# Kernel optimization log

Hardware: AMD Instinct MI355X
Metric: run time of the kernel (lower is better)

## Reference

```python
import jax, jax.numpy as jnp
import numpy as np
from jax import lax

D_MODEL = 768
D_STATE = 16
D_CONV = 4
EXPAND = 2
D_INNER = EXPAND * D_MODEL  # 1536
DT_RANK = (D_MODEL + 15) // 16  # 48
BATCH = 4
SEQ_LEN = 2048


def setup_inputs() -> dict:
    key = jax.random.key(0)
    ks = jax.random.split(key, 8)
    x = jax.random.normal(ks[0], (BATCH, SEQ_LEN, D_MODEL), dtype=jnp.float32)
    W_in = jax.random.normal(ks[1], (D_INNER * 2, D_MODEL), dtype=jnp.float32) * 0.02
    conv_w = jax.random.normal(ks[2], (D_INNER, 1, D_CONV), dtype=jnp.float32) * 0.1
    conv_b = jnp.zeros((D_INNER,), dtype=jnp.float32)
    W_x = jax.random.normal(ks[3], (DT_RANK + 2 * D_STATE, D_INNER), dtype=jnp.float32) * 0.02
    dt_std = DT_RANK ** -0.5
    W_dt = jax.random.uniform(ks[4], (D_INNER, DT_RANK), minval=-dt_std, maxval=dt_std, dtype=jnp.float32)
    b_dt = jnp.zeros((D_INNER,), dtype=jnp.float32)
    A_log = jnp.log(jnp.tile(jnp.arange(1, D_STATE + 1, dtype=jnp.float32), (D_INNER, 1)))
    D_param = jnp.ones((D_INNER,), dtype=jnp.float32)
    W_out = jax.random.normal(ks[5], (D_MODEL, D_INNER), dtype=jnp.float32) * 0.02
    return {"x": x, "W_in": W_in, "conv_w": conv_w, "conv_b": conv_b,
            "W_x": W_x, "W_dt": W_dt, "b_dt": b_dt, "A_log": A_log,
            "D_param": D_param, "W_out": W_out}


def _silu(v):
    return v * jax.nn.sigmoid(v)


def reference(x, W_in, conv_w, conv_b, W_x, W_dt, b_dt, A_log, D_param, W_out):
    B, L, _ = x.shape
    # in_proj and split into x-branch / gate z
    xz = jnp.einsum('bld,ed->ble', x, W_in)            # (B, L, 2*d_inner)
    xb, z = jnp.split(xz, 2, axis=-1)
    # depthwise causal conv1d (torch pads both sides then truncates to L)
    xc = jnp.transpose(xb, (0, 2, 1))                   # (B, d_inner, L)
    xc = lax.conv_general_dilated(xc, conv_w, window_strides=(1,),
                                  padding=[(D_CONV - 1, 0)],
                                  feature_group_count=D_INNER,
                                  dimension_numbers=('NCH', 'OIH', 'NCH'))
    xc = xc + conv_b[None, :, None]
    xc = jnp.transpose(xc, (0, 2, 1))                   # (B, L, d_inner)
    xc = _silu(xc)
    # ssm input-dependent params
    x_dbl = jnp.einsum('bld,ed->ble', xc, W_x)          # (B, L, dt_rank+2*d_state)
    dt_r = x_dbl[..., :DT_RANK]
    Bm = x_dbl[..., DT_RANK:DT_RANK + D_STATE]          # (B, L, d_state)
    Cm = x_dbl[..., DT_RANK + D_STATE:]
    dt = jax.nn.softplus(jnp.einsum('blr,dr->bld', dt_r, W_dt) + b_dt)
    A = -jnp.exp(A_log)                                 # (d_inner, d_state)
    # selective scan over time
    def step(h, inp):
        x_t, dt_t, B_t, C_t = inp                       # (B,d_inner),(B,d_inner),(B,d_state),(B,d_state)
        dA = jnp.exp(dt_t[..., None] * A)               # (B, d_inner, d_state)
        h = dA * h + (dt_t * x_t)[..., None] * B_t[:, None, :]
        y_t = jnp.einsum('bdn,bn->bd', h, C_t) + D_param * x_t
        return h, y_t
    h0 = jnp.zeros((B, D_INNER, D_STATE), dtype=x.dtype)
    xs = (jnp.transpose(xc, (1, 0, 2)), jnp.transpose(dt, (1, 0, 2)),
          jnp.transpose(Bm, (1, 0, 2)), jnp.transpose(Cm, (1, 0, 2)))
    _, ys = lax.scan(step, h0, xs)                      # (L, B, d_inner)
    y = jnp.transpose(ys, (1, 0, 2))
    y = y * _silu(z)
    return jnp.einsum('bld,od->blo', y, W_out)
```

## Files before the change

kernel.cpp:

```cpp
#include <hip/hip_runtime.h>
#include <hip/hip_bf16.h>
#include <math.h>

#define D_MODEL   768
#define D_STATE   16
#define D_CONV    4
#define D_INNER   1536
#define DT_RANK   48
#define BATCH     4
#define SEQ_LEN   2048
#define BL        (BATCH * SEQ_LEN)
#define NCHUNK    32
#define CHUNK     (SEQ_LEN / NCHUNK)

typedef __bf16 bf16x8 __attribute__((ext_vector_type(8)));
typedef float  f32x4  __attribute__((ext_vector_type(4)));

__device__ __forceinline__ void async_copy16(const void* g, void* l) {
    __builtin_amdgcn_global_load_lds(
        (const __attribute__((address_space(1))) void*)g,
        (__attribute__((address_space(3))) void*)l,
        16, 0, 0);
}

template <int EPI>
__global__ __launch_bounds__(256)
void gemm_f(const __bf16* __restrict__ A, const __bf16* __restrict__ B,
            float* __restrict__ C, const float* __restrict__ bias,
            int M, int N, int K, int ldc)
{
    __shared__ __bf16 Asl[128 * 64];
    __shared__ __bf16 Bsl[128 * 64];

    const int tid  = threadIdx.x;
    const int lane = tid & 63;
    const int w    = tid >> 6;
    const int wm   = (w >> 1) * 64;
    const int wn   = (w & 1) * 64;

    const int bm = blockIdx.y * 128;
    const int bn = blockIdx.x * 128;

    const long lda = 2L * K;
    const long ldb = 2L * K;

    f32x4 acc[4][4];
    #pragma unroll
    for (int i = 0; i < 4; ++i)
        #pragma unroll
        for (int j = 0; j < 4; ++j)
            acc[i][j] = (f32x4){0.f, 0.f, 0.f, 0.f};

    const int srow = w * 32 + (lane >> 3);
    const int q    = (lane & 7) ^ ((lane >> 3) & 7);
    const int qoff = (q < 4) ? q * 8 : K + (q - 4) * 8;
    const __bf16* Abase = A + (long)(bm + srow) * lda + qoff;
    const __bf16* Bbase = B + (long)(bn + srow) * ldb + qoff;
    char* AslW = (char*)Asl + (w * 32) * 128;
    char* BslW = (char*)Bsl + (w * 32) * 128;

    const int fr = lane & 15;
    const int g4 = lane >> 4;
    const long lda8 = 8 * lda, ldb8 = 8 * ldb;

    for (int kk = 0; kk < K; kk += 32) {
        __syncthreads();
        #pragma unroll
        for (int j = 0; j < 4; ++j) {
            async_copy16(Abase + j * lda8 + kk, AslW + j * 1024);
            async_copy16(Bbase + j * ldb8 + kk, BslW + j * 1024);
        }
        __syncthreads();

        bf16x8 ah[4], al[4], bh[4], bl[4];
        #pragma unroll
        for (int t = 0; t < 4; ++t) {
            const int ra = wm + t * 16 + fr;
            const int rb = wn + t * 16 + fr;
            ah[t] = *(const bf16x8*)&Asl[ra * 64 + ((g4       ^ (ra & 7)) * 8)];
            al[t] = *(const bf16x8*)&Asl[ra * 64 + (((4 + g4) ^ (ra & 7)) * 8)];
            bh[t] = *(const bf16x8*)&Bsl[rb * 64 + ((g4       ^ (rb & 7)) * 8)];
            bl[t] = *(const bf16x8*)&Bsl[rb * 64 + (((4 + g4) ^ (rb & 7)) * 8)];
        }
        #pragma unroll
        for (int i = 0; i < 4; ++i)
            #pragma unroll
            for (int j = 0; j < 4; ++j) {
                acc[i][j] = __builtin_amdgcn_mfma_f32_16x16x32_bf16(ah[i], bh[j], acc[i][j], 0, 0, 0);
                acc[i][j] = __builtin_amdgcn_mfma_f32_16x16x32_bf16(ah[i], bl[j], acc[i][j], 0, 0, 0);
                acc[i][j] = __builtin_amdgcn_mfma_f32_16x16x32_bf16(al[i], bh[j], acc[i][j], 0, 0, 0);
            }
    }

    const int cn  = lane & 15;
    const int cr4 = (lane >> 4) * 4;
    #pragma unroll
    for (int i = 0; i < 4; ++i)
        #pragma unroll
        for (int j = 0; j < 4; ++j)
            #pragma unroll
            for (int r = 0; r < 4; ++r) {
                const int row = bm + wm + i * 16 + cr4 + r;
                const int col = bn + wn + j * 16 + cn;
                float v = acc[i][j][r];
                if (EPI == 1) {
                    v += bias[col];
                    v = fmaxf(v, 0.f) + log1pf(__expf(-fabsf(v)));
                }
                C[(long)row * ldc + col] = v;
            }
}

__global__ __launch_bounds__(256)
void gemm_xdbl(const __bf16* __restrict__ A, const __bf16* __restrict__ B,
               float* __restrict__ Pout)
{
    __shared__ __bf16 Asl[128 * 64];
    __shared__ __bf16 Bsl[128 * 64];

    const int tid  = threadIdx.x;
    const int lane = tid & 63;
    const int w    = tid >> 6;
    const int wm   = (w >> 1) * 64;
    const int wn   = (w & 1) * 64;

    const int s  = blockIdx.x;
    const int bm = blockIdx.y * 128;
    const int K  = 1536;
    const long lda = 3072, ldb = 3072;

    f32x4 acc[4][4];
    #pragma unroll
    for (int i = 0; i < 4; ++i)
        #pragma unroll
        for (int j = 0; j < 4; ++j)
            acc[i][j] = (f32x4){0.f, 0.f, 0.f, 0.f};

    const int srow = w * 32 + (lane >> 3);
    const int q    = (lane & 7) ^ ((lane >> 3) & 7);
    const int qoff = (q < 4) ? q * 8 : K + (q - 4) * 8;
    const __bf16* Abase = A + (long)(bm + srow) * lda + qoff;
    const __bf16* Bbase = B + (long)srow * ldb + qoff;
    char* AslW = (char*)Asl + (w * 32) * 128;
    char* BslW = (char*)Bsl + (w * 32) * 128;

    const int fr = lane & 15;
    const int g4 = lane >> 4;
    const long lda8 = 8 * lda, ldb8 = 8 * ldb;

    for (int kt = s * 12; kt < (s + 1) * 12; ++kt) {
        const int kk = kt * 32;
        __syncthreads();
        #pragma unroll
        for (int j = 0; j < 4; ++j) {
            async_copy16(Abase + j * lda8 + kk, AslW + j * 1024);
            async_copy16(Bbase + j * ldb8 + kk, BslW + j * 1024);
        }
        __syncthreads();

        bf16x8 ah[4], al[4], bh[4], bl[4];
        #pragma unroll
        for (int t = 0; t < 4; ++t) {
            const int ra = wm + t * 16 + fr;
            const int rb = wn + t * 16 + fr;
            ah[t] = *(const bf16x8*)&Asl[ra * 64 + ((g4       ^ (ra & 7)) * 8)];
            al[t] = *(const bf16x8*)&Asl[ra * 64 + (((4 + g4) ^ (ra & 7)) * 8)];
            bh[t] = *(const bf16x8*)&Bsl[rb * 64 + ((g4       ^ (rb & 7)) * 8)];
            bl[t] = *(const bf16x8*)&Bsl[rb * 64 + (((4 + g4) ^ (rb & 7)) * 8)];
        }
        #pragma unroll
        for (int i = 0; i < 4; ++i)
            #pragma unroll
            for (int j = 0; j < 4; ++j) {
                acc[i][j] = __builtin_amdgcn_mfma_f32_16x16x32_bf16(ah[i], bh[j], acc[i][j], 0, 0, 0);
                acc[i][j] = __builtin_amdgcn_mfma_f32_16x16x32_bf16(ah[i], bl[j], acc[i][j], 0, 0, 0);
                acc[i][j] = __builtin_amdgcn_mfma_f32_16x16x32_bf16(al[i], bh[j], acc[i][j], 0, 0, 0);
            }
    }

    float* Cp = Pout + (long)s * (8192L * 128);
    const int cn  = lane & 15;
    const int cr4 = (lane >> 4) * 4;
    #pragma unroll
    for (int i = 0; i < 4; ++i)
        #pragma unroll
        for (int j = 0; j < 4; ++j)
            #pragma unroll
            for (int r = 0; r < 4; ++r) {
                const int row = bm + wm + i * 16 + cr4 + r;
                const int col = wn + j * 16 + cn;
                Cp[(long)row * 128 + col] = acc[i][j][r];
            }
}

__global__ __launch_bounds__(256)
void xdbl_reduce3(const float* __restrict__ Pout, float* __restrict__ xbc,
                  __bf16* __restrict__ xdtS)
{
    const long i = (long)blockIdx.x * 256 + threadIdx.x;
    if (i >= 8192L * 128) return;
    const long r  = i >> 7;
    const int  c  = (int)(i & 127);
    const long st = 8192L * 128;
    const long rb = r * 128;

    const int k = c & 63;
    float u = 0.f;
    if (k < 48) {
        const long o = rb + k;
        u = (Pout[o] + Pout[o + st]) + (Pout[o + 2 * st] + Pout[o + 3 * st]);
    }
    const __bf16 hi = (__bf16)u;
    xdtS[rb + c] = (c < 64) ? hi : (__bf16)(u - (float)hi);

    if (c >= 96) {
        const int j = c - 96;
        const long o = rb + 48 + j;
        xbc[r * 32 + j] =
            (Pout[o] + Pout[o + st]) + (Pout[o + 2 * st] + Pout[o + 3 * st]);
    }
}

#define NW0 ((long)BL * 768)
#define NW1 (3072L * 768)
#define NW2 (768L * 1536)
#define NW3 (80L * 1536)
#define NW4 (1536L * 128)
__global__ __launch_bounds__(256)
void split_all(const float* __restrict__ x,
               const float* __restrict__ W_in, const float* __restrict__ W_out,
               const float* __restrict__ W_x, const float* __restrict__ W_dt,
               __bf16* __restrict__ xS,
               __bf16* __restrict__ wInS, __bf16* __restrict__ wOutS,
               __bf16* __restrict__ wXS, __bf16* __restrict__ wDtS)
{
    long i = (long)blockIdx.x * 256 + threadIdx.x;
    if (i < NW0) {
        const long row = i / 768; const int col = (int)(i - row * 768);
        const float a = x[i];
        const __bf16 h = (__bf16)a;
        __bf16* d = xS + row * 1536 + col;
        d[0] = h; d[768] = (__bf16)(a - (float)h);
        return;
    }
    i -= NW0;
    if (i < NW1) {
        const long row = i / 768; const int col = (int)(i - row * 768);
        const float a = W_in[i];
        const __bf16 h = (__bf16)a;
        __bf16* d = wInS + row * 1536 + col;
        d[0] = h; d[768] = (__bf16)(a - (float)h);
        return;
    }
    i -= NW1;
    if (i < NW2) {
        const long row = i / 1536; const int col = (int)(i - row * 1536);
        const float a = W_out[i];
        const __bf16 h = (__bf16)a;
        __bf16* d = wOutS + row * 3072 + col;
        d[0] = h; d[1536] = (__bf16)(a - (float)h);
        return;
    }
    i -= NW2;
    if (i < NW3) {
        const long row = i / 1536; const int col = (int)(i - row * 1536);
        const float a = W_x[i];
        const __bf16 h = (__bf16)a;
        __bf16* d = wXS + row * 3072 + col;
        d[0] = h; d[1536] = (__bf16)(a - (float)h);
        return;
    }
    i -= NW3;
    if (i < NW4) {
        const long row = i >> 7; const int c = (int)(i & 127);
        const int k = c & 63;
        const float a = (k < 48) ? W_dt[row * 48 + k] : 0.f;
        const __bf16 h = (__bf16)a;
        wDtS[row * 128 + c] = (c < 64) ? h : (__bf16)(a - (float)h);
    }
}

__global__ __launch_bounds__(256)
void conv_silu_kernel(const float* __restrict__ xz,
                      const float* __restrict__ conv_w,
                      const float* __restrict__ conv_b,
                      __bf16* __restrict__ xcS)
{
    const long idx = (long)blockIdx.x * 256 + threadIdx.x;
    const int d  = (int)(idx % D_INNER);
    const long bl = idx / D_INNER;
    const int l  = (int)(bl % SEQ_LEN);

    const float w0 = conv_w[d * 4 + 0];
    const float w1 = conv_w[d * 4 + 1];
    const float w2 = conv_w[d * 4 + 2];
    const float w3 = conv_w[d * 4 + 3];

    const float* base = xz + bl * 3072 + d;
    float s = conv_b[d];
    if (l >= 3) s = fmaf(base[-3 * 3072], w0, s);
    if (l >= 2) s = fmaf(base[-2 * 3072], w1, s);
    if (l >= 1) s = fmaf(base[-1 * 3072], w2, s);
    s = fmaf(base[0], w3, s);
    const float sig = 1.f / (1.f + __expf(-s));
    const float v = s * sig;
    const __bf16 hi = (__bf16)v;
    const __bf16 lo = (__bf16)(v - (float)hi);
    xcS[bl * 3072 + d]        = hi;
    xcS[bl * 3072 + 1536 + d] = lo;
}

__global__ __launch_bounds__(256)
void scan_phaseA(const __bf16* __restrict__ xcS, const float* __restrict__ xz,
                 const float* __restrict__ xbc, const float* __restrict__ A_log,
                 float* __restrict__ P, float* __restrict__ S)
{
    const int d = blockIdx.x * 256 + threadIdx.x;
    const int c = blockIdx.y;
    const int b = blockIdx.z;

    float An[16], Pr[16], Sr[16];
    #pragma unroll
    for (int n = 0; n < 16; ++n) {
        An[n] = -__expf(A_log[d * 16 + n]);
        Pr[n] = 1.f;
        Sr[n] = 0.f;
    }

    const long bl0 = (long)b * SEQ_LEN + (long)c * CHUNK;
    for (int l = 0; l < CHUNK; ++l) {
        const long bl = bl0 + l;
        const float dt  = xz[bl * 3072 + d];
        const float x   = (float)xcS[bl * 3072 + d] + (float)xcS[bl * 3072 + 1536 + d];
        const float dtx = dt * x;
        const float* bc = xbc + bl * 32;
        #pragma unroll
        for (int n = 0; n < 16; ++n) {
            const float a = __expf(dt * An[n]);
            Pr[n] *= a;
            Sr[n] = fmaf(a, Sr[n], dtx * bc[n]);
        }
    }

    const long base = ((long)(b * NCHUNK + c) * 16) * D_INNER + d;
    #pragma unroll
    for (int n = 0; n < 16; ++n) {
        P[base + (long)n * D_INNER] = Pr[n];
        S[base + (long)n * D_INNER] = Sr[n];
    }
}

__global__ __launch_bounds__(256)
void scan_phaseB(const float* __restrict__ P, const float* __restrict__ S,
                 float* __restrict__ H)
{
    const int t = blockIdx.x * 256 + threadIdx.x;
    const int d = t % D_INNER;
    const int r = t / D_INNER;
    const int n = r & 15;
    const int b = r >> 4;

    float h = 0.f;
    for (int c = 0; c < NCHUNK; ++c) {
        const long i = ((long)(b * NCHUNK + c) * 16 + n) * D_INNER + d;
        H[i] = h;
        h = fmaf(P[i], h, S[i]);
    }
}

__global__ __launch_bounds__(256)
void scan_phaseC(__bf16* xcS_yS, const float* __restrict__ xz,
                 const float* __restrict__ xbc, const float* __restrict__ A_log,
                 const float* __restrict__ Dp, const float* __restrict__ H)
{
    const int d = blockIdx.x * 256 + threadIdx.x;
    const int c = blockIdx.y;
    const int b = blockIdx.z;

    float An[16], h[16];
    const long hbase = ((long)(b * NCHUNK + c) * 16) * D_INNER + d;
    #pragma unroll
    for (int n = 0; n < 16; ++n) {
        An[n] = -__expf(A_log[d * 16 + n]);
        h[n]  = H[hbase + (long)n * D_INNER];
    }
    const float Dd = Dp[d];

    const long bl0 = (long)b * SEQ_LEN + (long)c * CHUNK;
    for (int l = 0; l < CHUNK; ++l) {
        const long bl = bl0 + l;
        const float dt  = xz[bl * 3072 + d];
        const float x   = (float)xcS_yS[bl * 3072 + d] + (float)xcS_yS[bl * 3072 + 1536 + d];
        const float dtx = dt * x;
        const float* bc = xbc + bl * 32;
        float y = Dd * x;
        #pragma unroll
        for (int n = 0; n < 16; ++n) {
            const float a = __expf(dt * An[n]);
            h[n] = fmaf(a, h[n], dtx * bc[n]);
            y = fmaf(h[n], bc[16 + n], y);
        }
        const float z  = xz[bl * 3072 + D_INNER + d];
        const float sz = z / (1.f + __expf(-z));
        const float v  = y * sz;
        const __bf16 hi = (__bf16)v;
        const __bf16 lo = (__bf16)(v - (float)hi);
        xcS_yS[bl * 3072 + d]        = hi;
        xcS_yS[bl * 3072 + 1536 + d] = lo;
    }
}

extern "C" void kernel_launch(void* const* d_in, const int* in_sizes, int n_in,
                              void* d_out, int out_size, void* d_ws, size_t ws_size,
                              hipStream_t stream)
{
    const float* x      = (const float*)d_in[0];
    const float* W_in   = (const float*)d_in[1];
    const float* conv_w = (const float*)d_in[2];
    const float* conv_b = (const float*)d_in[3];
    const float* W_x    = (const float*)d_in[4];
    const float* W_dt   = (const float*)d_in[5];
    const float* b_dt   = (const float*)d_in[6];
    const float* A_log  = (const float*)d_in[7];
    const float* D_p    = (const float*)d_in[8];
    const float* W_out  = (const float*)d_in[9];
    float* out = (float*)d_out;

    char* p = (char*)d_ws;
    auto take = [&](size_t bytes) { char* r = p; p += (bytes + 255) & ~(size_t)255; return r; };

    float*  xz    = (float*)take((size_t)BL * 3072 * 4);
    float*  H     = (float*)take((size_t)BATCH * NCHUNK * 16 * D_INNER * 4);
    __bf16* wOutS = (__bf16*)take(768L * 3072 * 2);
    __bf16* wXS   = (__bf16*)take(128L * 3072 * 2);
    __bf16* wDtS  = (__bf16*)take(1536L * 128 * 2);
    __bf16* xdtS  = (__bf16*)take(8192L * 128 * 2);
    float*  xbc   = (float*)take(8192L * 32 * 4);
    float*  Pout  = (float*)take(4L * 8192 * 128 * 4);
    float*  S     = (float*)take((size_t)BATCH * NCHUNK * 16 * D_INNER * 4);
    float*  P     = Pout;

    char* region = take(50331648);
    __bf16* xS   = (__bf16*)region;
    __bf16* wInS = (__bf16*)(region + 25165824);
    __bf16* xcS  = (__bf16*)region;
    __bf16* yS   = (__bf16*)region;

    {
        const long n = NW0 + NW1 + NW2 + NW3 + NW4;
        split_all<<<(int)((n + 255) / 256), 256, 0, stream>>>(
            x, W_in, W_out, W_x, W_dt, xS, wInS, wOutS, wXS, wDtS);
    }
    {
        dim3 grid(3072 / 128, BL / 128);
        gemm_f<0><<<grid, 256, 0, stream>>>(xS, wInS, xz, nullptr,
                                            BL, 3072, 768, 3072);
    }
    {
        const long total = (long)BL * D_INNER;
        conv_silu_kernel<<<(int)(total / 256), 256, 0, stream>>>(xz, conv_w, conv_b, xcS);
    }
    {
        dim3 grid(4, BL / 128);
        gemm_xdbl<<<grid, 256, 0, stream>>>(xcS, wXS, Pout);
    }
    {
        const long n = 8192L * 128;
        xdbl_reduce3<<<(int)((n + 255) / 256), 256, 0, stream>>>(Pout, xbc, xdtS);
    }
    {
        dim3 grid(1536 / 128, BL / 128);
        gemm_f<1><<<grid, 256, 0, stream>>>(xdtS, wDtS, xz, b_dt,
                                            BL, 1536, 64, 3072);
    }
    {
        dim3 grid(D_INNER / 256, NCHUNK, BATCH);
        scan_phaseA<<<grid, 256, 0, stream>>>(xcS, xz, xbc, A_log, P, S);
    }
    scan_phaseB<<<(BATCH * 16 * D_INNER) / 256, 256, 0, stream>>>(P, S, H);
    {
        dim3 grid(D_INNER / 256, NCHUNK, BATCH);
        scan_phaseC<<<grid, 256, 0, stream>>>(xcS, xz, xbc, A_log, D_p, H);
    }
    {
        dim3 grid(768 / 128, BL / 128);
        gemm_f<0><<<grid, 256, 0, stream>>>(yS, wOutS, out, nullptr,
                                            BL, 768, 1536, 768);
    }
}
```

Baseline: 530.8 us.

## Double-buffer LDS tiles in split-bf16 GEMMs to overlap loads with MFMA

Both the generic GEMM and the x_dbl GEMM now use two LDS buffers, issuing async global-to-LDS copies for the next K-tile before running the MFMAs on the current one. The old sync-load-sync-compute pattern is replaced by a vmcnt wait plus a barrier, and s_setprio is raised around the MFMA block. The intent is to hide global load latency behind compute, at the cost of doubling LDS use (64KB per block), which may reduce occupancy. The loop assumes an even tile count.

```diff
diff --git a/kernel.cpp b/kernel.cpp
--- a/kernel.cpp
+++ b/kernel.cpp
@@ -23,14 +23,60 @@
         16, 0, 0);
 }
 
+
+#define TILE_SYNC() do {                                    \
+    asm volatile("s_waitcnt vmcnt(0)" ::: "memory");        \
+    __builtin_amdgcn_s_barrier();                           \
+} while (0)
+
+__device__ __forceinline__ void tile_stage(const __bf16* Ab, const __bf16* Bb,
+                                           long lda8, long ldb8, int kk,
+                                           char* AslW, char* BslW)
+{
+    #pragma unroll
+    for (int j = 0; j < 4; ++j) {
+        async_copy16(Ab + j * lda8 + kk, AslW + j * 1024);
+        async_copy16(Bb + j * ldb8 + kk, BslW + j * 1024);
+    }
+    __builtin_amdgcn_sched_barrier(0);
+}
+
+__device__ __forceinline__ void tile_compute(const __bf16* Asl, const __bf16* Bsl,
+                                             int wm, int wn, int fr, int g4,
+                                             f32x4 (&acc)[4][4])
+{
+    bf16x8 ah[4], al[4], bh[4], bl[4];
+    #pragma unroll
+    for (int t = 0; t < 4; ++t) {
+        const int ra = wm + t * 16 + fr;
+        const int rb = wn + t * 16 + fr;
+        ah[t] = *(const bf16x8*)&Asl[ra * 64 + ((g4       ^ (ra & 7)) * 8)];
+        al[t] = *(const bf16x8*)&Asl[ra * 64 + (((4 + g4) ^ (ra & 7)) * 8)];
+        bh[t] = *(const bf16x8*)&Bsl[rb * 64 + ((g4       ^ (rb & 7)) * 8)];
+        bl[t] = *(const bf16x8*)&Bsl[rb * 64 + (((4 + g4) ^ (rb & 7)) * 8)];
+    }
+    __builtin_amdgcn_s_setprio(1);
+    #pragma unroll
+    for (int i = 0; i < 4; ++i)
+        #pragma unroll
+        for (int j = 0; j < 4; ++j) {
+            acc[i][j] = __builtin_amdgcn_mfma_f32_16x16x32_bf16(ah[i], bh[j], acc[i][j], 0, 0, 0);
+            acc[i][j] = __builtin_amdgcn_mfma_f32_16x16x32_bf16(ah[i], bl[j], acc[i][j], 0, 0, 0);
+            acc[i][j] = __builtin_amdgcn_mfma_f32_16x16x32_bf16(al[i], bh[j], acc[i][j], 0, 0, 0);
+        }
+    __builtin_amdgcn_s_setprio(0);
+}
+
 template <int EPI>
 __global__ __launch_bounds__(256)
 void gemm_f(const __bf16* __restrict__ A, const __bf16* __restrict__ B,
             float* __restrict__ C, const float* __restrict__ bias,
             int M, int N, int K, int ldc)
 {
-    __shared__ __bf16 Asl[128 * 64];
-    __shared__ __bf16 Bsl[128 * 64];
+    __shared__ __bf16 Asl0[128 * 64];
+    __shared__ __bf16 Bsl0[128 * 64];
+    __shared__ __bf16 Asl1[128 * 64];
+    __shared__ __bf16 Bsl1[128 * 64];
 
     const int tid  = threadIdx.x;
     const int lane = tid & 63;
@@ -56,40 +102,29 @@
     const int qoff = (q < 4) ? q * 8 : K + (q - 4) * 8;
     const __bf16* Abase = A + (long)(bm + srow) * lda + qoff;
     const __bf16* Bbase = B + (long)(bn + srow) * ldb + qoff;
-    char* AslW = (char*)Asl + (w * 32) * 128;
-    char* BslW = (char*)Bsl + (w * 32) * 128;
+    const int wb = (w * 32) * 128;
+    char* AslW0 = (char*)Asl0 + wb;
+    char* BslW0 = (char*)Bsl0 + wb;
+    char* AslW1 = (char*)Asl1 + wb;
+    char* BslW1 = (char*)Bsl1 + wb;
 
     const int fr = lane & 15;
     const int g4 = lane >> 4;
     const long lda8 = 8 * lda, ldb8 = 8 * ldb;
 
-    for (int kk = 0; kk < K; kk += 32) {
-        __syncthreads();
-        #pragma unroll
-        for (int j = 0; j < 4; ++j) {
-            async_copy16(Abase + j * lda8 + kk, AslW + j * 1024);
-            async_copy16(Bbase + j * ldb8 + kk, BslW + j * 1024);
-        }
-        __syncthreads();
-
-        bf16x8 ah[4], al[4], bh[4], bl[4];
-        #pragma unroll
-        for (int t = 0; t < 4; ++t) {
-            const int ra = wm + t * 16 + fr;
-            const int rb = wn + t * 16 + fr;
-            ah[t] = *(const bf16x8*)&Asl[ra * 64 + ((g4       ^ (ra & 7)) * 8)];
-            al[t] = *(const bf16x8*)&Asl[ra * 64 + (((4 + g4) ^ (ra & 7)) * 8)];
-            bh[t] = *(const bf16x8*)&Bsl[rb * 64 + ((g4       ^ (rb & 7)) * 8)];
-            bl[t] = *(const bf16x8*)&Bsl[rb * 64 + (((4 + g4) ^ (rb & 7)) * 8)];
-        }
-        #pragma unroll
-        for (int i = 0; i < 4; ++i)
-            #pragma unroll
-            for (int j = 0; j < 4; ++j) {
-                acc[i][j] = __builtin_amdgcn_mfma_f32_16x16x32_bf16(ah[i], bh[j], acc[i][j], 0, 0, 0);
-                acc[i][j] = __builtin_amdgcn_mfma_f32_16x16x32_bf16(ah[i], bl[j], acc[i][j], 0, 0, 0);
-                acc[i][j] = __builtin_amdgcn_mfma_f32_16x16x32_bf16(al[i], bh[j], acc[i][j], 0, 0, 0);
-            }
+    const int nt = K >> 5;
+
+    tile_stage(Abase, Bbase, lda8, ldb8, 0, AslW0, BslW0);
+    TILE_SYNC();
+
+    for (int tt = 0; tt < nt; tt += 2) {
+        tile_stage(Abase, Bbase, lda8, ldb8, (tt + 1) * 32, AslW1, BslW1);
+        tile_compute(Asl0, Bsl0, wm, wn, fr, g4, acc);
+        TILE_SYNC();
+        if (tt + 2 < nt)
+            tile_stage(Abase, Bbase, lda8, ldb8, (tt + 2) * 32, AslW0, BslW0);
+        tile_compute(Asl1, Bsl1, wm, wn, fr, g4, acc);
+        TILE_SYNC();
     }
 
     const int cn  = lane & 15;
@@ -115,8 +150,10 @@
 void gemm_xdbl(const __bf16* __restrict__ A, const __bf16* __restrict__ B,
                float* __restrict__ Pout)
 {
-    __shared__ __bf16 Asl[128 * 64];
-    __shared__ __bf16 Bsl[128 * 64];
+    __shared__ __bf16 Asl0[128 * 64];
+    __shared__ __bf16 Bsl0[128 * 64];
+    __shared__ __bf16 Asl1[128 * 64];
+    __shared__ __bf16 Bsl1[128 * 64];
 
     const int tid  = threadIdx.x;
     const int lane = tid & 63;
@@ -141,41 +178,29 @@
     const int qoff = (q < 4) ? q * 8 : K + (q - 4) * 8;
     const __bf16* Abase = A + (long)(bm + srow) * lda + qoff;
     const __bf16* Bbase = B + (long)srow * ldb + qoff;
-    char* AslW = (char*)Asl + (w * 32) * 128;
-    char* BslW = (char*)Bsl + (w * 32) * 128;
+    const int wb = (w * 32) * 128;
+    char* AslW0 = (char*)Asl0 + wb;
+    char* BslW0 = (char*)Bsl0 + wb;
+    char* AslW1 = (char*)Asl1 + wb;
+    char* BslW1 = (char*)Bsl1 + wb;
 
     const int fr = lane & 15;
     const int g4 = lane >> 4;
     const long lda8 = 8 * lda, ldb8 = 8 * ldb;
 
-    for (int kt = s * 12; kt < (s + 1) * 12; ++kt) {
-        const int kk = kt * 32;
-        __syncthreads();
-        #pragma unroll
-        for (int j = 0; j < 4; ++j) {
-            async_copy16(Abase + j * lda8 + kk, AslW + j * 1024);
-            async_copy16(Bbase + j * ldb8 + kk, BslW + j * 1024);
-        }
-        __syncthreads();
-
-        bf16x8 ah[4], al[4], bh[4], bl[4];
-        #pragma unroll
-        for (int t = 0; t < 4; ++t) {
-            const int ra = wm + t * 16 + fr;
-            const int rb = wn + t * 16 + fr;
-            ah[t] = *(const bf16x8*)&Asl[ra * 64 + ((g4       ^ (ra & 7)) * 8)];
-            al[t] = *(const bf16x8*)&Asl[ra * 64 + (((4 + g4) ^ (ra & 7)) * 8)];
-            bh[t] = *(const bf16x8*)&Bsl[rb * 64 + ((g4       ^ (rb & 7)) * 8)];
-            bl[t] = *(const bf16x8*)&Bsl[rb * 64 + (((4 + g4) ^ (rb & 7)) * 8)];
-        }
-        #pragma unroll
-        for (int i = 0; i < 4; ++i)
-            #pragma unroll
-            for (int j = 0; j < 4; ++j) {
-                acc[i][j] = __builtin_amdgcn_mfma_f32_16x16x32_bf16(ah[i], bh[j], acc[i][j], 0, 0, 0);
-                acc[i][j] = __builtin_amdgcn_mfma_f32_16x16x32_bf16(ah[i], bl[j], acc[i][j], 0, 0, 0);
-                acc[i][j] = __builtin_amdgcn_mfma_f32_16x16x32_bf16(al[i], bh[j], acc[i][j], 0, 0, 0);
-            }
+    const int k0 = s * 384;
+
+    tile_stage(Abase, Bbase, lda8, ldb8, k0, AslW0, BslW0);
+    TILE_SYNC();
+
+    for (int tt = 0; tt < 12; tt += 2) {
+        tile_stage(Abase, Bbase, lda8, ldb8, k0 + (tt + 1) * 32, AslW1, BslW1);
+        tile_compute(Asl0, Bsl0, wm, wn, fr, g4, acc);
+        TILE_SYNC();
+        if (tt + 2 < 12)
+            tile_stage(Abase, Bbase, lda8, ldb8, k0 + (tt + 2) * 32, AslW0, BslW0);
+        tile_compute(Asl1, Bsl1, wm, wn, fr, g4, acc);
+        TILE_SYNC();
     }
 
     float* Cp = Pout + (long)s * (8192L * 128);
```

After: 533.4 us. About the same (+0.5%).

## Triple-buffer GEMM loads with 128x192 tiles, 8 waves, and grid swizzle

Applied to the files above, without the earlier changes.

Rewrites the generic split-bf16 GEMM to use a three-stage LDS ring buffer. Async global-to-LDS copies for tile t+2 are issued while tile t is computed, replacing the two-barrier load-then-compute loop. The block grows to 512 threads with a 128x192 output tile, uses a workgroup index swizzle for L2 locality, and raises wave priority around the MFMA block. This aims to hide global load latency and reduce barrier stalls, at the cost of more LDS (about 120 KB) and tighter register and occupancy limits.

```diff
diff --git a/kernel.cpp b/kernel.cpp
--- a/kernel.cpp
+++ b/kernel.cpp
@@ -24,72 +24,108 @@
 }
 
 template <int EPI>
-__global__ __launch_bounds__(256)
+__global__ __launch_bounds__(512, 2)
 void gemm_f(const __bf16* __restrict__ A, const __bf16* __restrict__ B,
             float* __restrict__ C, const float* __restrict__ bias,
             int M, int N, int K, int ldc)
 {
-    __shared__ __bf16 Asl[128 * 64];
-    __shared__ __bf16 Bsl[128 * 64];
+    __shared__ __bf16 Asl[3][128 * 64];
+    __shared__ __bf16 Bsl[3][192 * 64];
 
     const int tid  = threadIdx.x;
     const int lane = tid & 63;
     const int w    = tid >> 6;
-    const int wm   = (w >> 1) * 64;
-    const int wn   = (w & 1) * 64;
-
-    const int bm = blockIdx.y * 128;
-    const int bn = blockIdx.x * 128;
+    const int wm   = (w >> 2) * 64;
+    const int wn   = (w & 3) * 48;
+
+    const int nwg  = gridDim.x * gridDim.y;
+    const int orig = blockIdx.x + gridDim.x * blockIdx.y;
+    const int swz  = (orig & 7) * (nwg >> 3) + (orig >> 3);
+    const int bn   = (swz % gridDim.x) * 192;
+    const int bm   = (swz / gridDim.x) * 128;
 
     const long lda = 2L * K;
     const long ldb = 2L * K;
 
-    f32x4 acc[4][4];
+    f32x4 acc[4][3];
     #pragma unroll
     for (int i = 0; i < 4; ++i)
         #pragma unroll
-        for (int j = 0; j < 4; ++j)
+        for (int j = 0; j < 3; ++j)
             acc[i][j] = (f32x4){0.f, 0.f, 0.f, 0.f};
 
-    const int srow = w * 32 + (lane >> 3);
-    const int q    = (lane & 7) ^ ((lane >> 3) & 7);
+    const int srow = w * 8 + (lane >> 3);
+    const int q    = (lane & 7) ^ (lane >> 3);
     const int qoff = (q < 4) ? q * 8 : K + (q - 4) * 8;
     const __bf16* Abase = A + (long)(bm + srow) * lda + qoff;
     const __bf16* Bbase = B + (long)(bn + srow) * ldb + qoff;
-    char* AslW = (char*)Asl + (w * 32) * 128;
-    char* BslW = (char*)Bsl + (w * 32) * 128;
+    const long lda64 = 64 * lda, ldb64 = 64 * ldb;
+    const int wboff = w * 1024;
 
     const int fr = lane & 15;
     const int g4 = lane >> 4;
-    const long lda8 = 8 * lda, ldb8 = 8 * ldb;
-
-    for (int kk = 0; kk < K; kk += 32) {
-        __syncthreads();
-        #pragma unroll
-        for (int j = 0; j < 4; ++j) {
-            async_copy16(Abase + j * lda8 + kk, AslW + j * 1024);
-            async_copy16(Bbase + j * ldb8 + kk, BslW + j * 1024);
-        }
-        __syncthreads();
-
-        bf16x8 ah[4], al[4], bh[4], bl[4];
+
+    const int nt = K >> 5;
+
+    auto STAGE = [&](int kk, int buf) {
+        char* Ad = (char*)Asl[buf] + wboff;
+        char* Bd = (char*)Bsl[buf] + wboff;
+        async_copy16(Abase + kk,             Ad);
+        async_copy16(Abase + kk + lda64,     Ad + 8192);
+        async_copy16(Bbase + kk,             Bd);
+        async_copy16(Bbase + kk + ldb64,     Bd + 8192);
+        async_copy16(Bbase + kk + 2 * ldb64, Bd + 16384);
+    };
+
+    auto COMPUTE = [&](int buf) {
+        const __bf16* As = Asl[buf];
+        const __bf16* Bs = Bsl[buf];
+        bf16x8 ah[4], al[4], bh[3], bl[3];
         #pragma unroll
         for (int t = 0; t < 4; ++t) {
             const int ra = wm + t * 16 + fr;
+            ah[t] = *(const bf16x8*)&As[ra * 64 + ((g4       ^ (ra & 7)) * 8)];
+            al[t] = *(const bf16x8*)&As[ra * 64 + (((4 + g4) ^ (ra & 7)) * 8)];
+        }
+        #pragma unroll
+        for (int t = 0; t < 3; ++t) {
             const int rb = wn + t * 16 + fr;
-            ah[t] = *(const bf16x8*)&Asl[ra * 64 + ((g4       ^ (ra & 7)) * 8)];
-            al[t] = *(const bf16x8*)&Asl[ra * 64 + (((4 + g4) ^ (ra & 7)) * 8)];
-            bh[t] = *(const bf16x8*)&Bsl[rb * 64 + ((g4       ^ (rb & 7)) * 8)];
-            bl[t] = *(const bf16x8*)&Bsl[rb * 64 + (((4 + g4) ^ (rb & 7)) * 8)];
+            bh[t] = *(const bf16x8*)&Bs[rb * 64 + ((g4       ^ (rb & 7)) * 8)];
+            bl[t] = *(const bf16x8*)&Bs[rb * 64 + (((4 + g4) ^ (rb & 7)) * 8)];
         }
+        __builtin_amdgcn_s_setprio(1);
         #pragma unroll
         for (int i = 0; i < 4; ++i)
             #pragma unroll
-            for (int j = 0; j < 4; ++j) {
+            for (int j = 0; j < 3; ++j) {
                 acc[i][j] = __builtin_amdgcn_mfma_f32_16x16x32_bf16(ah[i], bh[j], acc[i][j], 0, 0, 0);
                 acc[i][j] = __builtin_amdgcn_mfma_f32_16x16x32_bf16(ah[i], bl[j], acc[i][j], 0, 0, 0);
                 acc[i][j] = __builtin_amdgcn_mfma_f32_16x16x32_bf16(al[i], bh[j], acc[i][j], 0, 0, 0);
             }
+        __builtin_amdgcn_s_setprio(0);
+    };
+
+    auto ITER = [&](int t, int cb, int sb) {
+        if (t + 2 < nt) STAGE((t + 2) * 32, sb);
+        __builtin_amdgcn_sched_barrier(0);
+        COMPUTE(cb);
+        asm volatile("s_waitcnt lgkmcnt(0)" ::: "memory");
+        if (t + 2 < nt) asm volatile("s_waitcnt vmcnt(5)" ::: "memory");
+        else            asm volatile("s_waitcnt vmcnt(0)" ::: "memory");
+        __builtin_amdgcn_s_barrier();
+        __builtin_amdgcn_sched_barrier(0);
+    };
+
+    STAGE(0, 0);
+    STAGE(32, 1);
+    asm volatile("s_waitcnt vmcnt(5)" ::: "memory");
+    __builtin_amdgcn_s_barrier();
+    __builtin_amdgcn_sched_barrier(0);
+
+    for (int t = 0; t < nt; t += 3) {
+        ITER(t, 0, 2);
+        if (t + 1 < nt) ITER(t + 1, 1, 0);
+        if (t + 2 < nt) ITER(t + 2, 2, 1);
     }
 
     const int cn  = lane & 15;
@@ -97,7 +133,7 @@
     #pragma unroll
     for (int i = 0; i < 4; ++i)
         #pragma unroll
-        for (int j = 0; j < 4; ++j)
+        for (int j = 0; j < 3; ++j)
             #pragma unroll
             for (int r = 0; r < 4; ++r) {
                 const int row = bm + wm + i * 16 + cr4 + r;
@@ -452,8 +488,8 @@
             x, W_in, W_out, W_x, W_dt, xS, wInS, wOutS, wXS, wDtS);
     }
     {
-        dim3 grid(3072 / 128, BL / 128);
-        gemm_f<0><<<grid, 256, 0, stream>>>(xS, wInS, xz, nullptr,
+        dim3 grid(3072 / 192, BL / 128);
+        gemm_f<0><<<grid, 512, 0, stream>>>(xS, wInS, xz, nullptr,
                                             BL, 3072, 768, 3072);
     }
     {
@@ -469,8 +505,8 @@
         xdbl_reduce3<<<(int)((n + 255) / 256), 256, 0, stream>>>(Pout, xbc, xdtS);
     }
     {
-        dim3 grid(1536 / 128, BL / 128);
-        gemm_f<1><<<grid, 256, 0, stream>>>(xdtS, wDtS, xz, b_dt,
+        dim3 grid(1536 / 192, BL / 128);
+        gemm_f<1><<<grid, 512, 0, stream>>>(xdtS, wDtS, xz, b_dt,
                                             BL, 1536, 64, 3072);
     }
     {
@@ -483,8 +519,8 @@
         scan_phaseC<<<grid, 256, 0, stream>>>(xcS, xz, xbc, A_log, D_p, H);
     }
     {
-        dim3 grid(768 / 128, BL / 128);
-        gemm_f<0><<<grid, 256, 0, stream>>>(yS, wOutS, out, nullptr,
+        dim3 grid(768 / 192, BL / 128);
+        gemm_f<0><<<grid, 512, 0, stream>>>(yS, wOutS, out, nullptr,
                                             BL, 768, 1536, 768);
     }
 }
```

Result: slower. 548.6 us (+3.3%).

## Replace in_proj GEMM with 256x256-tile 8-wave double-buffered split-bf16 kernel

Applied to the files above, without the earlier changes.

Adds a new GEMM kernel for the in_proj matmul that uses 256x256 output tiles with 512 threads, double-buffered LDS filled by async global-to-LDS copies, and quarter-step interleaving of loads with MFMA work under fine-grained vmcnt waits and s_setprio. It keeps the three-product hi/lo bf16 split for near-fp32 accuracy. The larger tile is meant to raise arithmetic intensity and overlap memory with MFMA. In exchange it uses 128KB of LDS and many accumulator registers, which limits occupancy, and its epilogue does scalar stores.

```diff
diff --git a/kernel.cpp b/kernel.cpp
--- a/kernel.cpp
+++ b/kernel.cpp
@@ -21,6 +21,171 @@
         (const __attribute__((address_space(1))) void*)g,
         (__attribute__((address_space(3))) void*)l,
         16, 0, 0);
+}
+
+
+#define SYNC_V4 do { asm volatile("s_waitcnt vmcnt(4)" ::: "memory"); \
+    __builtin_amdgcn_s_barrier(); __builtin_amdgcn_sched_barrier(0); } while (0)
+#define SYNC_V2 do { asm volatile("s_waitcnt vmcnt(2)" ::: "memory"); \
+    __builtin_amdgcn_s_barrier(); __builtin_amdgcn_sched_barrier(0); } while (0)
+#define SYNC_V0 do { asm volatile("s_waitcnt vmcnt(0)" ::: "memory"); \
+    __builtin_amdgcn_s_barrier(); __builtin_amdgcn_sched_barrier(0); } while (0)
+
+template<int IH, int JH>
+__device__ __forceinline__ void quad24(f32x4 (&acc)[2][4][2][2],
+                                       const bf16x8 (&aH)[4], const bf16x8 (&aL)[4],
+                                       const bf16x8 (&bH)[2], const bf16x8 (&bL)[2])
+{
+    __builtin_amdgcn_s_setprio(1);
+    #pragma unroll
+    for (int i = 0; i < 4; ++i)
+        #pragma unroll
+        for (int j = 0; j < 2; ++j) {
+            acc[IH][i][JH][j] = __builtin_amdgcn_mfma_f32_16x16x32_bf16(aH[i], bH[j], acc[IH][i][JH][j], 0, 0, 0);
+            acc[IH][i][JH][j] = __builtin_amdgcn_mfma_f32_16x16x32_bf16(aH[i], bL[j], acc[IH][i][JH][j], 0, 0, 0);
+            acc[IH][i][JH][j] = __builtin_amdgcn_mfma_f32_16x16x32_bf16(aL[i], bH[j], acc[IH][i][JH][j], 0, 0, 0);
+        }
+    __builtin_amdgcn_s_setprio(0);
+}
+
+__global__ __launch_bounds__(512, 2)
+void gemm256(const __bf16* __restrict__ A, const __bf16* __restrict__ B,
+             float* __restrict__ C, int K, int ldc)
+{
+    __shared__ __bf16 Asl0[256 * 64];
+    __shared__ __bf16 Bsl0[256 * 64];
+    __shared__ __bf16 Asl1[256 * 64];
+    __shared__ __bf16 Bsl1[256 * 64];
+
+    const int tid  = threadIdx.x;
+    const int lane = tid & 63;
+    const int w    = tid >> 6;
+    const int aw   = (w >> 2) * 64;
+    const int bw   = (w & 3) * 32;
+
+    const int bm = blockIdx.y * 256;
+    const int bn = blockIdx.x * 256;
+
+    const long lda = 2L * K;
+    const long ldb = 2L * K;
+
+    f32x4 acc[2][4][2][2];
+    #pragma unroll
+    for (int a = 0; a < 2; ++a)
+        #pragma unroll
+        for (int i = 0; i < 4; ++i)
+            #pragma unroll
+            for (int b = 0; b < 2; ++b)
+                #pragma unroll
+                for (int j = 0; j < 2; ++j)
+                    acc[a][i][b][j] = (f32x4){0.f, 0.f, 0.f, 0.f};
+
+    const int srow = w * 8 + (lane >> 3);
+    const int q    = (lane & 7) ^ ((lane >> 3) & 7);
+    const int qoff = (q < 4) ? q * 8 : K + (q - 4) * 8;
+    const __bf16* Ab = A + (long)(bm + srow) * lda + qoff;
+    const __bf16* Bb = B + (long)(bn + srow) * ldb + qoff;
+    const long lda64 = 64 * lda, ldb64 = 64 * ldb;
+    const int wo = w * 1024;
+
+    const int fr = lane & 15;
+    const int g4 = lane >> 4;
+
+    const int nt = K >> 5;
+
+    __bf16 *Ac = Asl0, *Bc = Bsl0, *An = Asl1, *Bn = Bsl1;
+
+    auto stA = [&](int kk, __bf16* dst, int half) {
+        char* d = (char*)dst + half * 16384 + wo;
+        const __bf16* s = Ab + kk + (long)(2 * half) * lda64;
+        async_copy16(s, d);
+        async_copy16(s + lda64, d + 8192);
+    };
+    auto stB = [&](int kk, __bf16* dst, int half) {
+        char* d = (char*)dst + half * 16384 + wo;
+        const __bf16* s = Bb + kk + (long)(2 * half) * ldb64;
+        async_copy16(s, d);
+        async_copy16(s + ldb64, d + 8192);
+    };
+    auto rdA = [&](const __bf16* As, int ih, bf16x8 (&aH)[4], bf16x8 (&aL)[4]) {
+        #pragma unroll
+        for (int t = 0; t < 4; ++t) {
+            const int ra = aw + ih * 128 + t * 16 + fr;
+            aH[t] = *(const bf16x8*)&As[ra * 64 + ((g4       ^ (ra & 7)) * 8)];
+            aL[t] = *(const bf16x8*)&As[ra * 64 + (((4 + g4) ^ (ra & 7)) * 8)];
+        }
+    };
+    auto rdB = [&](const __bf16* Bs, int jh, bf16x8 (&bH)[2], bf16x8 (&bL)[2]) {
+        #pragma unroll
+        for (int t = 0; t < 2; ++t) {
+            const int rb = bw + jh * 128 + t * 16 + fr;
+            bH[t] = *(const bf16x8*)&Bs[rb * 64 + ((g4       ^ (rb & 7)) * 8)];
+            bL[t] = *(const bf16x8*)&Bs[rb * 64 + (((4 + g4) ^ (rb & 7)) * 8)];
+        }
+    };
+
+    stA(0, Ac, 0);
+    stB(0, Bc, 0);
+    stB(0, Bc, 1);
+    stA(0, Ac, 1);
+    SYNC_V4;
+
+    for (int t = 0; t < nt - 1; ++t) {
+        const int kk1 = (t + 1) * 32;
+        bf16x8 aH[4], aL[4], bH[2], bL[2];
+        rdA(Ac, 0, aH, aL);
+        rdB(Bc, 0, bH, bL);
+        stA(kk1, An, 0);
+        SYNC_V4;
+        quad24<0, 0>(acc, aH, aL, bH, bL);
+        rdB(Bc, 1, bH, bL);
+        stB(kk1, Bn, 0);
+        SYNC_V4;
+        quad24<0, 1>(acc, aH, aL, bH, bL);
+        rdA(Ac, 1, aH, aL);
+        stB(kk1, Bn, 1);
+        SYNC_V4;
+        quad24<1, 1>(acc, aH, aL, bH, bL);
+        rdB(Bc, 0, bH, bL);
+        stA(kk1, An, 1);
+        SYNC_V4;
+        quad24<1, 0>(acc, aH, aL, bH, bL);
+        __bf16* tp;
+        tp = Ac; Ac = An; An = tp;
+        tp = Bc; Bc = Bn; Bn = tp;
+    }
+
+    {
+        bf16x8 aH[4], aL[4], bH[2], bL[2];
+        rdA(Ac, 0, aH, aL);
+        rdB(Bc, 0, bH, bL);
+        SYNC_V2;
+        quad24<0, 0>(acc, aH, aL, bH, bL);
+        rdB(Bc, 1, bH, bL);
+        SYNC_V0;
+        quad24<0, 1>(acc, aH, aL, bH, bL);
+        rdA(Ac, 1, aH, aL);
+        quad24<1, 1>(acc, aH, aL, bH, bL);
+        rdB(Bc, 0, bH, bL);
+        quad24<1, 0>(acc, aH, aL, bH, bL);
+    }
+
+    const int cn  = lane & 15;
+    const int cr4 = (lane >> 4) * 4;
+    #pragma unroll
+    for (int ih = 0; ih < 2; ++ih)
+        #pragma unroll
+        for (int i = 0; i < 4; ++i)
+            #pragma unroll
+            for (int jh = 0; jh < 2; ++jh)
+                #pragma unroll
+                for (int j = 0; j < 2; ++j)
+                    #pragma unroll
+                    for (int r = 0; r < 4; ++r) {
+                        const int row = bm + aw + ih * 128 + i * 16 + cr4 + r;
+                        const int col = bn + bw + jh * 128 + j * 16 + cn;
+                        C[(long)row * ldc + col] = acc[ih][i][jh][j][r];
+                    }
 }
 
 template <int EPI>
@@ -452,9 +617,8 @@
             x, W_in, W_out, W_x, W_dt, xS, wInS, wOutS, wXS, wDtS);
     }
     {
-        dim3 grid(3072 / 128, BL / 128);
-        gemm_f<0><<<grid, 256, 0, stream>>>(xS, wInS, xz, nullptr,
-                                            BL, 3072, 768, 3072);
+        dim3 grid(3072 / 256, BL / 256);
+        gemm256<<<grid, 512, 0, stream>>>(xS, wInS, xz, 768, 3072);
     }
     {
         const long total = (long)BL * D_INNER;
```

After: 524.2 us. No clear change (-1.2%).
